# Kernel tuning notes

Hardware: AMD Instinct MI355X
Metric: run time of the kernel (lower is better)

The kernel has to match this reference:

```python
import jax, jax.numpy as jnp
import numpy as np

B, A, G = 16, 32, 512      # batch, atoms, g_feat_in
S, M = 1024, 8             # subset samples, peaks per subset
E, OH = 5, 20              # element types, thermometer size per element
FE = E * OH                # formula encoding = 100
D = 512                    # internal_d
NBINS = 512                # spect bins
EPS = 1e-4


def _ln(x, g, b):
    m = x.mean(-1, keepdims=True)
    v = jnp.mean((x - m) ** 2, -1, keepdims=True)
    return (x - m) * jax.lax.rsqrt(v + 1e-5) * g + b


def setup_inputs() -> dict:
    key = jax.random.key(0)
    ks = jax.random.split(key, 16)
    vert_feat_in = jax.random.normal(ks[0], (B, A, G), jnp.float32)
    vert_mask_in = jnp.ones((B, A), jnp.float32)
    elem = jax.random.randint(ks[1], (B, A), 0, E)
    vert_element_oh = jax.nn.one_hot(elem, E, dtype=jnp.float32)
    atom_subsets = jax.random.randint(ks[2], (B, S, A), 0, 2).astype(jnp.int32)
    atom_subsets_peaks_mass_idx = jax.random.randint(ks[3], (B, S, M), 0, NBINS).astype(jnp.int32)
    atom_subsets_peaks_intensity = jax.random.uniform(ks[4], (B, S, M), jnp.float32)

    def lin(k, o, i):
        s = 1.0 / np.sqrt(i)
        return jax.random.uniform(k, (o, i), jnp.float32, -s, s)

    return dict(
        vert_feat_in=vert_feat_in, vert_mask_in=vert_mask_in,
        vert_element_oh=vert_element_oh, atom_subsets=atom_subsets,
        atom_subsets_peaks_mass_idx=atom_subsets_peaks_mass_idx,
        atom_subsets_peaks_intensity=atom_subsets_peaks_intensity,
        ln_sub_g=jnp.ones((G,)), ln_sub_b=jnp.zeros((G,)),
        W_ih=lin(ks[5], 3 * G, FE), W_hh=lin(ks[6], 3 * G, G),
        b_ih=jnp.zeros((3 * G,)), b_hh=jnp.zeros((3 * G,)),
        ln_post_g=jnp.ones((G,)), ln_post_b=jnp.zeros((G,)),
        W1=lin(ks[7], D, G), b1=jnp.zeros((D,)),
        W2a=lin(ks[8], D, D), b2a=jnp.zeros((D,)),
        W2b=lin(ks[9], D, D), b2b=jnp.zeros((D,)),
        ln_pre_g=jnp.ones((D,)), ln_pre_b=jnp.zeros((D,)),
        W_s=lin(ks[10], 1, D), b_s=jnp.zeros((1,)),
    )


def reference(vert_feat_in, vert_mask_in, vert_element_oh, atom_subsets,
              atom_subsets_peaks_mass_idx, atom_subsets_peaks_intensity,
              ln_sub_g, ln_sub_b, W_ih, W_hh, b_ih, b_hh,
              ln_post_g, ln_post_b, W1, b1, W2a, b2a, W2b, b2b,
              ln_pre_g, ln_pre_b, W_s, b_s):
    subs_f = atom_subsets.astype(jnp.float32)
    masked_vert = vert_feat_in * vert_mask_in[:, :, None]          # B,A,G
    subs_masked = subs_f * vert_mask_in[:, None, :]                 # B,S,A
    # subset-weighted pooling of vertex features
    swv_sum = jnp.einsum('baf,bsa->bsf', masked_vert, subs_masked)  # B,S,G
    subset_size = subs_masked.sum(-1) + EPS                         # B,S
    swv_mean = swv_sum / subset_size[..., None]
    h = _ln(swv_mean, ln_sub_g, ln_sub_b)                           # B,S,G
    # formula counts -> thermometer (accumulating) one-hot; .byte() cast kills grads
    counts = jax.lax.stop_gradient(
        jnp.einsum('bae,bsa->bse', vert_element_oh, subs_f))        # B,S,E
    therm = (jnp.arange(OH, dtype=jnp.float32)[None, None, None, :] < counts[..., None])
    formulae = therm.astype(jnp.float32).reshape(counts.shape[0], counts.shape[1], FE)
    # GRUCell: input=formula encoding, hidden=subset_normed
    gi = jnp.einsum('bsf,gf->bsg', formulae, W_ih) + b_ih           # B,S,3G
    gh = jnp.einsum('bsh,gh->bsg', h, W_hh) + b_hh
    gi_r, gi_z, gi_n = jnp.split(gi, 3, axis=-1)
    gh_r, gh_z, gh_n = jnp.split(gh, 3, axis=-1)
    r = jax.nn.sigmoid(gi_r + gh_r)
    z = jax.nn.sigmoid(gi_z + gh_z)
    n = jnp.tanh(gi_n + r * gh_n)
    combined = (1.0 - z) * n + z * h                                # B,S,G
    x = _ln(combined, ln_post_g, ln_post_b)
    x = jax.nn.relu(jnp.einsum('bsg,dg->bsd', x, W1) + b1)
    x = jax.nn.relu(jnp.einsum('bsd,ed->bse', x, W2a) + b2a)
    x = jax.nn.relu(jnp.einsum('bsd,ed->bse', x, W2b) + b2b)
    x = _ln(x, ln_pre_g, ln_pre_b)
    scores = (jnp.einsum('bsd,od->bso', x, W_s) + b_s)[..., 0]      # B,S
    probs = jax.nn.softmax(scores, axis=-1)                         # B,S
    # sparse mass-matrix multiply: scatter subset probs into spectrum bins
    weighted = atom_subsets_peaks_intensity * probs[:, :, None]     # B,S,M
    bidx = jnp.arange(probs.shape[0])[:, None, None]
    spect_out = jnp.zeros((probs.shape[0], NBINS), probs.dtype)
    spect_out = spect_out.at[bidx, atom_subsets_peaks_mass_idx].add(weighted)
    return spect_out, probs
```

## Files before the change

kernel.cpp:

```cpp
#include <hip/hip_runtime.h>

#define NB 16
#define NA 32
#define NG 512
#define NS 1024
#define NM 8
#define NE 5
#define NOH 20
#define NFE 100
#define ND 512
#define NBINS 512
#define NTOK (NB * NS)

typedef unsigned short ushort_t;
typedef __attribute__((ext_vector_type(8))) short bf16x8;
typedef __attribute__((ext_vector_type(4))) float f32x4;

__device__ __forceinline__ ushort_t f2bf(float x) {
  union { float f; unsigned u; } v; v.f = x;
  unsigned r = v.u + 0x7FFF + ((v.u >> 16) & 1);
  return (ushort_t)(r >> 16);
}
__device__ __forceinline__ float bf2f(ushort_t b) {
  union { unsigned u; float f; } v; v.u = ((unsigned)b) << 16;
  return v.f;
}

__device__ __forceinline__ void gload_lds16(const void* g, void* l) {
  __builtin_amdgcn_global_load_lds(
      (const __attribute__((address_space(1))) void*)g,
      (__attribute__((address_space(3))) void*)l, 16, 0, 0);
}

__device__ __forceinline__ float wsum64(float v) {
#pragma unroll
  for (int off = 32; off > 0; off >>= 1) v += __shfl_xor(v, off);
  return v;
}

__device__ __forceinline__ float fsig(float x) {
  return __builtin_amdgcn_rcpf(1.f + __expf(-x));
}
__device__ __forceinline__ float ftanh(float x) {
  float t = fminf(fmaxf(x, -15.f), 15.f);
  return 1.f - 2.f * __builtin_amdgcn_rcpf(__expf(2.f * t) + 1.f);
}

__global__ __launch_bounds__(256) void setup_kernel(
    const float* __restrict__ vert, const float* __restrict__ mask,
    const float* __restrict__ eloh, const int* __restrict__ subs,
    const float* __restrict__ Wih, const float* __restrict__ Whh,
    const float* __restrict__ W1, const float* __restrict__ W2a,
    const float* __restrict__ W2b,
    float* __restrict__ tcd, float* __restrict__ PS,
    ushort_t* __restrict__ o_hh, ushort_t* __restrict__ o1,
    ushort_t* __restrict__ o2a, ushort_t* __restrict__ o2b,
    ushort_t* __restrict__ VmT, ushort_t* __restrict__ S_bf) {
  int i = blockIdx.x * 256 + threadIdx.x;
  if (i < NTOK) {
    int b = i >> 10;
    const int* srow = subs + (size_t)i * NA;
    float cnt[NE] = {0.f, 0.f, 0.f, 0.f, 0.f};
    float z = 0.f;
    for (int a = 0; a < NA; a++) {
      float sb = (float)srow[a];
      z += sb * mask[b * NA + a];
      const float* eo = eloh + (size_t)(b * NA + a) * NE;
#pragma unroll
      for (int e = 0; e < NE; e++) cnt[e] += eo[e] * sb;
    }
    float* o = tcd + (size_t)i * 8;
#pragma unroll
    for (int e = 0; e < NE; e++) o[e] = cnt[e];
    o[5] = 1.0f / (z + 1e-4f);
    return;
  }
  i -= NTOK;
  if (i < NE * 1536) {
    int e = i / 1536, g = i % 1536;
    float s = 0.f;
    float* base = PS + ((size_t)e * 21) * 1536 + g;
    base[0] = 0.f;
    for (int c = 1; c <= NOH; c++) {
      s += Wih[(size_t)g * NFE + e * NOH + (c - 1)];
      base[(size_t)c * 1536] = s;
    }
    return;
  }
  i -= NE * 1536;
  if (i < 1536 * NG) { o_hh[i] = f2bf(Whh[i]); return; }
  i -= 1536 * NG;
  if (i < ND * NG) { o1[i] = f2bf(W1[i]); return; }
  i -= ND * NG;
  if (i < ND * ND) { o2a[i] = f2bf(W2a[i]); return; }
  i -= ND * ND;
  if (i < ND * ND) { o2b[i] = f2bf(W2b[i]); return; }
  i -= ND * ND;
  const int nV = NB * NG * NA;
  if (i < nV) {
    int b = i / (NG * NA); int rem = i % (NG * NA);
    int f = rem >> 5, a = rem & 31;
    float mk = mask[b * NA + a];
    VmT[i] = f2bf(vert[(size_t)b * NA * NG + a * NG + f] * mk * mk);
    return;
  }
  i -= nV;
  if (i < NTOK * NA) S_bf[i] = f2bf((float)subs[i]);
}

__global__ __launch_bounds__(256) void pool_gemm(
    const ushort_t* __restrict__ S_bf, const ushort_t* __restrict__ VmT,
    const float* __restrict__ tcd, float* __restrict__ SWV, int tok0) {
  __shared__ ushort_t As[128 * 32];
  __shared__ ushort_t Bs[128 * 32];
  const int t = threadIdx.x;
  const int w = t >> 6, lane = t & 63;
  const int wr = w >> 1, wc = w & 1;
  const int bm = blockIdx.x * 128;
  const int bn = blockIdx.y * 128;
  const int b = (tok0 + bm) >> 10;
  const int srow = lane >> 2;
  const int scol = (((lane & 3) ^ ((lane >> 3) & 3)) * 8);
  const ushort_t* Bbase = VmT + (size_t)b * NG * NA;
  gload_lds16(S_bf + (size_t)(tok0 + bm + w * 16 + srow) * 32 + scol, &As[w * 512]);
  gload_lds16(S_bf + (size_t)(tok0 + bm + 64 + w * 16 + srow) * 32 + scol, &As[2048 + w * 512]);
  gload_lds16(Bbase + (size_t)(bn + w * 16 + srow) * 32 + scol, &Bs[w * 512]);
  gload_lds16(Bbase + (size_t)(bn + 64 + w * 16 + srow) * 32 + scol, &Bs[2048 + w * 512]);
  __syncthreads();

  const int lr = lane & 15, lq = lane >> 4;
  const int rchunk = (lq ^ ((lr >> 1) & 3)) * 8;
  f32x4 acc[4][4];
#pragma unroll
  for (int m = 0; m < 4; m++)
#pragma unroll
    for (int n = 0; n < 4; n++) acc[m][n] = (f32x4)0.f;
  bf16x8 a[4], bb[4];
#pragma unroll
  for (int m = 0; m < 4; m++)
    a[m] = *(const bf16x8*)&As[(wr * 64 + m * 16 + lr) * 32 + rchunk];
#pragma unroll
  for (int n = 0; n < 4; n++)
    bb[n] = *(const bf16x8*)&Bs[(wc * 64 + n * 16 + lr) * 32 + rchunk];
#pragma unroll
  for (int m = 0; m < 4; m++)
#pragma unroll
    for (int n = 0; n < 4; n++)
      acc[m][n] = __builtin_amdgcn_mfma_f32_16x16x32_bf16(a[m], bb[n], acc[m][n], 0, 0, 0);

#pragma unroll
  for (int n = 0; n < 4; n++) {
    const int col = bn + wc * 64 + n * 16 + lr;
#pragma unroll
    for (int m = 0; m < 4; m++) {
      f32x4 v = acc[m][n];
#pragma unroll
      for (int r = 0; r < 4; r++) {
        int row = bm + wr * 64 + m * 16 + lq * 4 + r;
        float inv = tcd[(size_t)(tok0 + row) * 8 + 5];
        SWV[(size_t)row * NG + col] = v[r] * inv;
      }
    }
  }
}

__global__ __launch_bounds__(256) void finish_kernel(
    const float* __restrict__ SWV, const float* __restrict__ lng,
    const float* __restrict__ lnb, ushort_t* __restrict__ Hb) {
  const int t = threadIdx.x;
  const int lane = t & 63, wv = t >> 6;
  const int ltok = blockIdx.x * 4 + wv;
  const int f = lane * 8;
  const float* row = SWV + (size_t)ltok * NG + f;
  float4 v0 = *(const float4*)row;
  float4 v1 = *(const float4*)(row + 4);
  float x[8] = {v0.x, v0.y, v0.z, v0.w, v1.x, v1.y, v1.z, v1.w};
  float ps = 0.f;
#pragma unroll
  for (int j = 0; j < 8; j++) ps += x[j];
  float mean = wsum64(ps) * (1.0f / NG);
  float pq = 0.f;
#pragma unroll
  for (int j = 0; j < 8; j++) { float d = x[j] - mean; pq += d * d; }
  float rstd = rsqrtf(wsum64(pq) * (1.0f / NG) + 1e-5f);
  float4 g0 = *(const float4*)&lng[f], g1 = *(const float4*)&lng[f + 4];
  float4 b0 = *(const float4*)&lnb[f], b1 = *(const float4*)&lnb[f + 4];
  float gg[8] = {g0.x, g0.y, g0.z, g0.w, g1.x, g1.y, g1.z, g1.w};
  float bbv[8] = {b0.x, b0.y, b0.z, b0.w, b1.x, b1.y, b1.z, b1.w};
  bf16x8 ho;
#pragma unroll
  for (int j = 0; j < 8; j++) ho[j] = (short)f2bf((x[j] - mean) * rstd * gg[j] + bbv[j]);
  *(bf16x8*)&Hb[(size_t)ltok * NG + f] = ho;
}

__global__ __launch_bounds__(256) void gemm_bf16(
    const ushort_t* __restrict__ A, const ushort_t* __restrict__ W,
    const float* __restrict__ bias, ushort_t* __restrict__ C,
    int K, int Dout, int mode) {
  __shared__ ushort_t As[2][4096];
  __shared__ ushort_t Bs[2][4096];
  const int t = threadIdx.x;
  const int w = t >> 6;
  const int lane = t & 63;
  const int wr = w >> 1, wc = w & 1;
  const int bm = blockIdx.x * 128, bn = blockIdx.y * 128;

  const int srow = lane >> 2;
  const int scol = (((lane & 3) ^ ((lane >> 3) & 3)) * 8);
  const ushort_t* Ag0 = A + (size_t)(bm + w * 16 + srow) * K + scol;
  const ushort_t* Ag1 = A + (size_t)(bm + 64 + w * 16 + srow) * K + scol;
  const ushort_t* Wg0 = W + (size_t)(bn + w * 16 + srow) * K + scol;
  const ushort_t* Wg1 = W + (size_t)(bn + 64 + w * 16 + srow) * K + scol;
  const int l0 = w * 512;
  const int l1 = 2048 + w * 512;

  const int lr = lane & 15;
  const int lq = lane >> 4;
  const int rchunk = (lq ^ ((lr >> 1) & 3)) * 8;

  f32x4 acc[4][4];
#pragma unroll
  for (int m = 0; m < 4; m++)
#pragma unroll
    for (int n = 0; n < 4; n++) acc[m][n] = (f32x4)0.f;

  gload_lds16(Ag0, &As[0][l0]);
  gload_lds16(Ag1, &As[0][l1]);
  gload_lds16(Wg0, &Bs[0][l0]);
  gload_lds16(Wg1, &Bs[0][l1]);
  __syncthreads();

  const int nk = K >> 5;
  int cur = 0;
  for (int kt = 0; kt < nk; kt++) {
    if (kt + 1 < nk) {
      const int k1 = (kt + 1) << 5;
      gload_lds16(Ag0 + k1, &As[cur ^ 1][l0]);
      gload_lds16(Ag1 + k1, &As[cur ^ 1][l1]);
      gload_lds16(Wg0 + k1, &Bs[cur ^ 1][l0]);
      gload_lds16(Wg1 + k1, &Bs[cur ^ 1][l1]);
    }
    bf16x8 a[4], b[4];
#pragma unroll
    for (int m = 0; m < 4; m++)
      a[m] = *(const bf16x8*)&As[cur][(wr * 64 + m * 16 + lr) * 32 + rchunk];
#pragma unroll
    for (int n = 0; n < 4; n++)
      b[n] = *(const bf16x8*)&Bs[cur][(wc * 64 + n * 16 + lr) * 32 + rchunk];
#pragma unroll
    for (int m = 0; m < 4; m++)
#pragma unroll
      for (int n = 0; n < 4; n++)
        acc[m][n] = __builtin_amdgcn_mfma_f32_16x16x32_bf16(a[m], b[n], acc[m][n], 0, 0, 0);
    __syncthreads();
    cur ^= 1;
  }

  ushort_t* sc = (w < 2) ? &As[w][0] : &Bs[w - 2][0];
#pragma unroll
  for (int n = 0; n < 4; n++) {
    const float bv = bias[bn + wc * 64 + n * 16 + lr];
#pragma unroll
    for (int m = 0; m < 4; m++) {
      f32x4 v = acc[m][n];
#pragma unroll
      for (int r = 0; r < 4; r++) {
        const int row = m * 16 + lq * 4 + r;
        float u = v[r] + bv;
        if (mode == 1) u = fmaxf(u, 0.f);
        sc[row * 64 + ((n * 16 + lr) ^ ((row & 7) << 3))] = f2bf(u);
      }
    }
  }
  __builtin_amdgcn_s_waitcnt(0);
#pragma unroll
  for (int p = 0; p < 8; p++) {
    const int row = p * 8 + (lane >> 3);
    bf16x8 pk = *(const bf16x8*)&sc[row * 64 + (((lane & 7) * 8) ^ ((row & 7) << 3))];
    *(bf16x8*)&C[(size_t)(bm + wr * 64 + row) * Dout + bn + wc * 64 + (lane & 7) * 8] = pk;
  }
}

__global__ __launch_bounds__(256) void gate_ln_kernel(
    const ushort_t* __restrict__ Gh, const ushort_t* __restrict__ Hb,
    const float* __restrict__ tcd, const float* __restrict__ PS,
    const float* __restrict__ b_ih, const float* __restrict__ lng,
    const float* __restrict__ lnb, ushort_t* __restrict__ X0) {
  const int t = threadIdx.x;
  const int lane = t & 63, wv = t >> 6;
  const int ltok = blockIdx.x * 4 + wv;
  const int f = lane * 8;
  int c[NE];
#pragma unroll
  for (int e = 0; e < NE; e++) {
    int ci = (int)tcd[(size_t)ltok * 8 + e];
    c[e] = ci > NOH ? NOH : ci;
  }
  float4 r0 = *(const float4*)&b_ih[f],          r1 = *(const float4*)&b_ih[f + 4];
  float4 z0 = *(const float4*)&b_ih[NG + f],     z1 = *(const float4*)&b_ih[NG + f + 4];
  float4 n0 = *(const float4*)&b_ih[2 * NG + f], n1 = *(const float4*)&b_ih[2 * NG + f + 4];
#pragma unroll
  for (int e = 0; e < NE; e++) {
    const float* pe = PS + ((size_t)(e * 21 + c[e])) * 1536;
    r0 += *(const float4*)&pe[f];          r1 += *(const float4*)&pe[f + 4];
    z0 += *(const float4*)&pe[NG + f];     z1 += *(const float4*)&pe[NG + f + 4];
    n0 += *(const float4*)&pe[2 * NG + f]; n1 += *(const float4*)&pe[2 * NG + f + 4];
  }
  float gir[8] = {r0.x, r0.y, r0.z, r0.w, r1.x, r1.y, r1.z, r1.w};
  float giz[8] = {z0.x, z0.y, z0.z, z0.w, z1.x, z1.y, z1.z, z1.w};
  float gin[8] = {n0.x, n0.y, n0.z, n0.w, n1.x, n1.y, n1.z, n1.w};

  const ushort_t* gh = Gh + (size_t)ltok * 1536;
  bf16x8 vr = *(const bf16x8*)&gh[f];
  bf16x8 vz = *(const bf16x8*)&gh[NG + f];
  bf16x8 vn = *(const bf16x8*)&gh[2 * NG + f];
  bf16x8 vh = *(const bf16x8*)&Hb[(size_t)ltok * NG + f];
  float cv[8];
  float ps = 0.f;
#pragma unroll
  for (int j = 0; j < 8; j++) {
    float rg = fsig(gir[j] + bf2f((ushort_t)vr[j]));
    float zg = fsig(giz[j] + bf2f((ushort_t)vz[j]));
    float ng = ftanh(gin[j] + rg * bf2f((ushort_t)vn[j]));
    cv[j] = (1.f - zg) * ng + zg * bf2f((ushort_t)vh[j]);
    ps += cv[j];
  }
  float mean = wsum64(ps) * (1.0f / NG);
  float pq = 0.f;
#pragma unroll
  for (int j = 0; j < 8; j++) { float d = cv[j] - mean; pq += d * d; }
  float rstd = rsqrtf(wsum64(pq) * (1.0f / NG) + 1e-5f);
  float4 g0 = *(const float4*)&lng[f], g1 = *(const float4*)&lng[f + 4];
  float4 b0 = *(const float4*)&lnb[f], b1 = *(const float4*)&lnb[f + 4];
  float gg[8] = {g0.x, g0.y, g0.z, g0.w, g1.x, g1.y, g1.z, g1.w};
  float bbv[8] = {b0.x, b0.y, b0.z, b0.w, b1.x, b1.y, b1.z, b1.w};
  bf16x8 xo;
#pragma unroll
  for (int j = 0; j < 8; j++) xo[j] = (short)f2bf((cv[j] - mean) * rstd * gg[j] + bbv[j]);
  *(bf16x8*)&X0[(size_t)ltok * NG + f] = xo;
}

__global__ __launch_bounds__(256) void ln_score_kernel(
    const ushort_t* __restrict__ X, const float* __restrict__ lng,
    const float* __restrict__ lnb, const float* __restrict__ Wsc,
    const float* __restrict__ bsc, float* __restrict__ scores) {
  const int t = threadIdx.x;
  const int lane = t & 63, wv = t >> 6;
  const int ltok = blockIdx.x * 4 + wv;
  const int f = lane * 8;
  bf16x8 xx = *(const bf16x8*)&X[(size_t)ltok * ND + f];
  float x[8];
  float ps = 0.f;
#pragma unroll
  for (int j = 0; j < 8; j++) { x[j] = bf2f((ushort_t)xx[j]); ps += x[j]; }
  float mean = wsum64(ps) * (1.0f / ND);
  float pq = 0.f;
#pragma unroll
  for (int j = 0; j < 8; j++) { float d = x[j] - mean; pq += d * d; }
  float rstd = rsqrtf(wsum64(pq) * (1.0f / ND) + 1e-5f);
  float4 g0 = *(const float4*)&lng[f], g1 = *(const float4*)&lng[f + 4];
  float4 b0 = *(const float4*)&lnb[f], b1 = *(const float4*)&lnb[f + 4];
  float4 w0 = *(const float4*)&Wsc[f], w1 = *(const float4*)&Wsc[f + 4];
  float gg[8] = {g0.x, g0.y, g0.z, g0.w, g1.x, g1.y, g1.z, g1.w};
  float bbv[8] = {b0.x, b0.y, b0.z, b0.w, b1.x, b1.y, b1.z, b1.w};
  float ww[8] = {w0.x, w0.y, w0.z, w0.w, w1.x, w1.y, w1.z, w1.w};
  float d = 0.f;
#pragma unroll
  for (int j = 0; j < 8; j++) d += ((x[j] - mean) * rstd * gg[j] + bbv[j]) * ww[j];
  float dot = wsum64(d);
  if (lane == 0) scores[ltok] = dot + bsc[0];
}

__global__ __launch_bounds__(256) void softmax_scatter_kernel(
    const float* __restrict__ scores, const int* __restrict__ pidx,
    const float* __restrict__ pint, float* __restrict__ spect,
    float* __restrict__ probs) {
  const int b = blockIdx.x;
  const int t = threadIdx.x;
  __shared__ float s_red[4];
  __shared__ float s_spec[NBINS];
  const float* sc = scores + (size_t)b * NS;
  float v[4];
  float mx = -1e30f;
#pragma unroll
  for (int i = 0; i < 4; i++) { v[i] = sc[t + i * 256]; mx = fmaxf(mx, v[i]); }
#pragma unroll
  for (int off = 32; off > 0; off >>= 1) mx = fmaxf(mx, __shfl_down(mx, off));
  if ((t & 63) == 0) s_red[t >> 6] = mx;
  __syncthreads();
  mx = fmaxf(fmaxf(s_red[0], s_red[1]), fmaxf(s_red[2], s_red[3]));
  float e[4], sum = 0.f;
#pragma unroll
  for (int i = 0; i < 4; i++) { e[i] = expf(v[i] - mx); sum += e[i]; }
#pragma unroll
  for (int off = 32; off > 0; off >>= 1) sum += __shfl_down(sum, off);
  __syncthreads();
  if ((t & 63) == 0) s_red[t >> 6] = sum;
  __syncthreads();
  sum = s_red[0] + s_red[1] + s_red[2] + s_red[3];
  float inv = 1.f / sum;
  s_spec[t] = 0.f; s_spec[t + 256] = 0.f;
  float p[4];
#pragma unroll
  for (int i = 0; i < 4; i++) {
    p[i] = e[i] * inv;
    probs[(size_t)b * NS + t + i * 256] = p[i];
  }
  __syncthreads();
#pragma unroll
  for (int i = 0; i < 4; i++) {
    const int s = t + i * 256;
    const int* idx = pidx + ((size_t)b * NS + s) * NM;
    const float* wt = pint + ((size_t)b * NS + s) * NM;
#pragma unroll
    for (int m = 0; m < NM; m++)
      atomicAdd(&s_spec[idx[m]], wt[m] * p[i]);
  }
  __syncthreads();
  spect[(size_t)b * NBINS + t] = s_spec[t];
  spect[(size_t)b * NBINS + t + 256] = s_spec[t + 256];
}

extern "C" void kernel_launch(void* const* d_in, const int* in_sizes, int n_in,
                              void* d_out, int out_size, void* d_ws, size_t ws_size,
                              hipStream_t stream) {
  const float* vert = (const float*)d_in[0];
  const float* mask = (const float*)d_in[1];
  const float* eloh = (const float*)d_in[2];
  const int* subs = (const int*)d_in[3];
  const int* pidx = (const int*)d_in[4];
  const float* pint = (const float*)d_in[5];
  const float* ln_sub_g = (const float*)d_in[6];
  const float* ln_sub_b = (const float*)d_in[7];
  const float* W_ih = (const float*)d_in[8];
  const float* W_hh = (const float*)d_in[9];
  const float* b_ih = (const float*)d_in[10];
  const float* b_hh = (const float*)d_in[11];
  const float* ln_post_g = (const float*)d_in[12];
  const float* ln_post_b = (const float*)d_in[13];
  const float* W1 = (const float*)d_in[14];
  const float* b1 = (const float*)d_in[15];
  const float* W2a = (const float*)d_in[16];
  const float* b2a = (const float*)d_in[17];
  const float* W2b = (const float*)d_in[18];
  const float* b2b = (const float*)d_in[19];
  const float* ln_pre_g = (const float*)d_in[20];
  const float* ln_pre_b = (const float*)d_in[21];
  const float* W_s = (const float*)d_in[22];
  const float* b_s = (const float*)d_in[23];

  float* out = (float*)d_out;
  float* probs = out + NB * NBINS;

  char* ws = (char*)d_ws;
  float* scores = (float*)ws;
  ushort_t* Whh_bf = (ushort_t*)(ws + 65536);
  ushort_t* W1_bf  = (ushort_t*)(ws + 1638400);
  ushort_t* W2a_bf = (ushort_t*)(ws + 2162688);
  ushort_t* W2b_bf = (ushort_t*)(ws + 2686976);
  ushort_t* VmT    = (ushort_t*)(ws + 3211264);
  ushort_t* S_bf   = (ushort_t*)(ws + 3735552);
  float*    tcd    = (float*)(ws + 4784128);
  float*    PS     = (float*)(ws + 5308416);
  const size_t fixed = 5953536;

  const size_t per_tok = 7168;
  int T = NTOK;
  while (T > 1024 && fixed + (size_t)T * per_tok > ws_size) T >>= 1;
  const int nchunks = NTOK / T;

  char* cb = ws + fixed;
  float*    SWV = (float*)cb;                             cb += (size_t)T * 2048;
  ushort_t* Hb  = (ushort_t*)cb;                          cb += (size_t)T * 1024;
  ushort_t* Gh  = (ushort_t*)cb;                          cb += (size_t)T * 3072;
  ushort_t* X0  = (ushort_t*)cb;
  ushort_t* X1  = Gh;
  ushort_t* X2  = Gh + (size_t)T * 512;
  ushort_t* X3  = X0;

  const int setup_items = NTOK + NE * 1536 + 1536 * NG + ND * NG + 2 * ND * ND
                        + NB * NG * NA + NTOK * NA;
  setup_kernel<<<(setup_items + 255) / 256, 256, 0, stream>>>(
      vert, mask, eloh, subs, W_ih, W_hh, W1, W2a, W2b,
      tcd, PS, Whh_bf, W1_bf, W2a_bf, W2b_bf, VmT, S_bf);

  for (int c = 0; c < nchunks; c++) {
    const int tok0 = c * T;

    dim3 gp(T / 128, NG / 128);
    pool_gemm<<<gp, 256, 0, stream>>>(S_bf, VmT, tcd, SWV, tok0);
    finish_kernel<<<T / 4, 256, 0, stream>>>(SWV, ln_sub_g, ln_sub_b, Hb);

    dim3 g1(T / 128, 1536 / 128);
    gemm_bf16<<<g1, 256, 0, stream>>>(Hb, Whh_bf, b_hh, Gh, NG, 1536, 3);

    gate_ln_kernel<<<T / 4, 256, 0, stream>>>(Gh, Hb, tcd + (size_t)tok0 * 8, PS,
                                              b_ih, ln_post_g, ln_post_b, X0);

    dim3 g2(T / 128, ND / 128);
    gemm_bf16<<<g2, 256, 0, stream>>>(X0, W1_bf, b1, X1, NG, ND, 1);
    gemm_bf16<<<g2, 256, 0, stream>>>(X1, W2a_bf, b2a, X2, ND, ND, 1);
    gemm_bf16<<<g2, 256, 0, stream>>>(X2, W2b_bf, b2b, X3, ND, ND, 1);

    ln_score_kernel<<<T / 4, 256, 0, stream>>>(X3, ln_pre_g, ln_pre_b, W_s, b_s,
                                               scores + tok0);
  }

  softmax_scatter_kernel<<<NB, 256, 0, stream>>>(scores, pidx, pint, out, probs);
}
```

Measured before the change: 263.4 us.

## Fuse three FFN GEMMs and final LayerNorm-score into one LDS-resident kernel

Replaces the three separate bf16 GEMM launches and the ln_score kernel with a single kernel. Each 512-thread block keeps a 64-token activation tile in two swizzled LDS buffers and runs all three 512x512 layers back to back, with MFMA operands read from LDS and weights streamed from global memory. The final LayerNorm and score dot product are computed from LDS. This removes the global round trips of the intermediate activations and three launches. The cost is 128KB of LDS per block, so only one block fits per CU, and T/64 blocks may give low occupancy with weights reloaded by every block.

Measured after the change: 264.5 us. No clear change (+0.4%).

```diff
diff --git a/kernel.cpp b/kernel.cpp
--- a/kernel.cpp
+++ b/kernel.cpp
@@ -340,35 +340,106 @@
   *(bf16x8*)&X0[(size_t)ltok * NG + f] = xo;
 }
 
-__global__ __launch_bounds__(256) void ln_score_kernel(
-    const ushort_t* __restrict__ X, const float* __restrict__ lng,
+__device__ __forceinline__ void ffn_layer(
+    const ushort_t* src, ushort_t* dst, const ushort_t* __restrict__ Wl,
+    const float* __restrict__ bl, const int w, const int lane) {
+  const int lr = lane & 15, lq = lane >> 4;
+  const int cw = w * 64;
+  const int sw = lr & 7;
+  f32x4 acc[4][4];
+#pragma unroll
+  for (int m = 0; m < 4; m++)
+#pragma unroll
+    for (int n = 0; n < 4; n++) acc[m][n] = (f32x4)0.f;
+  const ushort_t* wp0 = Wl + (size_t)(cw + 0 + lr) * 512 + lq * 8;
+  const ushort_t* wp1 = Wl + (size_t)(cw + 16 + lr) * 512 + lq * 8;
+  const ushort_t* wp2 = Wl + (size_t)(cw + 32 + lr) * 512 + lq * 8;
+  const ushort_t* wp3 = Wl + (size_t)(cw + 48 + lr) * 512 + lq * 8;
+#pragma unroll
+  for (int kt = 0; kt < 16; kt++) {
+    bf16x8 a[4], b[4];
+    const int ch = (kt * 4 + lq) ^ sw;
+#pragma unroll
+    for (int m = 0; m < 4; m++)
+      a[m] = *(const bf16x8*)&src[(m * 16 + lr) * 512 + ch * 8];
+    b[0] = *(const bf16x8*)(wp0 + kt * 32);
+    b[1] = *(const bf16x8*)(wp1 + kt * 32);
+    b[2] = *(const bf16x8*)(wp2 + kt * 32);
+    b[3] = *(const bf16x8*)(wp3 + kt * 32);
+#pragma unroll
+    for (int m = 0; m < 4; m++)
+#pragma unroll
+      for (int n = 0; n < 4; n++)
+        acc[m][n] = __builtin_amdgcn_mfma_f32_16x16x32_bf16(a[m], b[n], acc[m][n], 0, 0, 0);
+  }
+#pragma unroll
+  for (int n = 0; n < 4; n++) {
+    const int c = cw + n * 16 + lr;
+    const float bv = bl[c];
+#pragma unroll
+    for (int m = 0; m < 4; m++) {
+      f32x4 v = acc[m][n];
+#pragma unroll
+      for (int r = 0; r < 4; r++) {
+        const int row = m * 16 + lq * 4 + r;
+        float u = fmaxf(v[r] + bv, 0.f);
+        dst[row * 512 + (((c >> 3) ^ (row & 7)) << 3) + (c & 7)] = f2bf(u);
+      }
+    }
+  }
+}
+
+__global__ __launch_bounds__(512) void ffn_kernel(
+    const ushort_t* __restrict__ X0g, const ushort_t* __restrict__ W1l,
+    const float* __restrict__ b1l, const ushort_t* __restrict__ W2al,
+    const float* __restrict__ b2al, const ushort_t* __restrict__ W2bl,
+    const float* __restrict__ b2bl, const float* __restrict__ lng,
     const float* __restrict__ lnb, const float* __restrict__ Wsc,
-    const float* __restrict__ bsc, float* __restrict__ scores) {
+    const float* __restrict__ bsc, float* __restrict__ scores, int tok0) {
+  __shared__ ushort_t Xa[64 * 512];
+  __shared__ ushort_t Xb[64 * 512];
   const int t = threadIdx.x;
-  const int lane = t & 63, wv = t >> 6;
-  const int ltok = blockIdx.x * 4 + wv;
-  const int f = lane * 8;
-  bf16x8 xx = *(const bf16x8*)&X[(size_t)ltok * ND + f];
-  float x[8];
-  float ps = 0.f;
-#pragma unroll
-  for (int j = 0; j < 8; j++) { x[j] = bf2f((ushort_t)xx[j]); ps += x[j]; }
-  float mean = wsum64(ps) * (1.0f / ND);
-  float pq = 0.f;
-#pragma unroll
-  for (int j = 0; j < 8; j++) { float d = x[j] - mean; pq += d * d; }
-  float rstd = rsqrtf(wsum64(pq) * (1.0f / ND) + 1e-5f);
-  float4 g0 = *(const float4*)&lng[f], g1 = *(const float4*)&lng[f + 4];
-  float4 b0 = *(const float4*)&lnb[f], b1 = *(const float4*)&lnb[f + 4];
-  float4 w0 = *(const float4*)&Wsc[f], w1 = *(const float4*)&Wsc[f + 4];
-  float gg[8] = {g0.x, g0.y, g0.z, g0.w, g1.x, g1.y, g1.z, g1.w};
-  float bbv[8] = {b0.x, b0.y, b0.z, b0.w, b1.x, b1.y, b1.z, b1.w};
-  float ww[8] = {w0.x, w0.y, w0.z, w0.w, w1.x, w1.y, w1.z, w1.w};
-  float d = 0.f;
-#pragma unroll
-  for (int j = 0; j < 8; j++) d += ((x[j] - mean) * rstd * gg[j] + bbv[j]) * ww[j];
-  float dot = wsum64(d);
-  if (lane == 0) scores[ltok] = dot + bsc[0];
+  const int w = t >> 6, lane = t & 63;
+  const int tb = blockIdx.x * 64;
+#pragma unroll
+  for (int i = 0; i < 8; i++) {
+    const int row = i * 8 + w;
+    gload_lds16(X0g + (size_t)(tok0 + tb + row) * 512 + ((lane ^ w) << 3),
+                &Xa[i * 4096 + w * 512]);
+  }
+  __syncthreads();
+  ffn_layer(Xa, Xb, W1l, b1l, w, lane);
+  __syncthreads();
+  ffn_layer(Xb, Xa, W2al, b2al, w, lane);
+  __syncthreads();
+  ffn_layer(Xa, Xb, W2bl, b2bl, w, lane);
+  __syncthreads();
+#pragma unroll
+  for (int j = 0; j < 8; j++) {
+    const int row = w * 8 + j;
+    bf16x8 xx = *(const bf16x8*)&Xb[row * 512 + ((lane ^ (row & 7)) << 3)];
+    float x[8];
+    float ps = 0.f;
+#pragma unroll
+    for (int q = 0; q < 8; q++) { x[q] = bf2f((ushort_t)xx[q]); ps += x[q]; }
+    float mean = wsum64(ps) * (1.0f / ND);
+    float pq = 0.f;
+#pragma unroll
+    for (int q = 0; q < 8; q++) { float d = x[q] - mean; pq += d * d; }
+    float rstd = rsqrtf(wsum64(pq) * (1.0f / ND) + 1e-5f);
+    const int f = lane * 8;
+    float4 g0 = *(const float4*)&lng[f], g1 = *(const float4*)&lng[f + 4];
+    float4 e0 = *(const float4*)&lnb[f], e1 = *(const float4*)&lnb[f + 4];
+    float4 s0 = *(const float4*)&Wsc[f], s1 = *(const float4*)&Wsc[f + 4];
+    float gg[8] = {g0.x, g0.y, g0.z, g0.w, g1.x, g1.y, g1.z, g1.w};
+    float bv[8] = {e0.x, e0.y, e0.z, e0.w, e1.x, e1.y, e1.z, e1.w};
+    float ww[8] = {s0.x, s0.y, s0.z, s0.w, s1.x, s1.y, s1.z, s1.w};
+    float d = 0.f;
+#pragma unroll
+    for (int q = 0; q < 8; q++) d += ((x[q] - mean) * rstd * gg[q] + bv[q]) * ww[q];
+    float dot = wsum64(d);
+    if (lane == 0) scores[tok0 + tb + row] = dot + bsc[0];
+  }
 }
 
 __global__ __launch_bounds__(256) void softmax_scatter_kernel(
@@ -474,9 +545,6 @@
   ushort_t* Hb  = (ushort_t*)cb;                          cb += (size_t)T * 1024;
   ushort_t* Gh  = (ushort_t*)cb;                          cb += (size_t)T * 3072;
   ushort_t* X0  = (ushort_t*)cb;
-  ushort_t* X1  = Gh;
-  ushort_t* X2  = Gh + (size_t)T * 512;
-  ushort_t* X3  = X0;
 
   const int setup_items = NTOK + NE * 1536 + 1536 * NG + ND * NG + 2 * ND * ND
                         + NB * NG * NA + NTOK * NA;
@@ -497,13 +565,8 @@
     gate_ln_kernel<<<T / 4, 256, 0, stream>>>(Gh, Hb, tcd + (size_t)tok0 * 8, PS,
                                               b_ih, ln_post_g, ln_post_b, X0);
 
-    dim3 g2(T / 128, ND / 128);
-    gemm_bf16<<<g2, 256, 0, stream>>>(X0, W1_bf, b1, X1, NG, ND, 1);
-    gemm_bf16<<<g2, 256, 0, stream>>>(X1, W2a_bf, b2a, X2, ND, ND, 1);
-    gemm_bf16<<<g2, 256, 0, stream>>>(X2, W2b_bf, b2b, X3, ND, ND, 1);
-
-    ln_score_kernel<<<T / 4, 256, 0, stream>>>(X3, ln_pre_g, ln_pre_b, W_s, b_s,
-                                               scores + tok0);
+    ffn_kernel<<<T / 64, 512, 0, stream>>>(X0, W1_bf, b1, W2a_bf, b2a, W2b_bf, b2b,
+                                           ln_pre_g, ln_pre_b, W_s, b_s, scores, tok0);
   }
 
   softmax_scatter_kernel<<<NB, 256, 0, stream>>>(scores, pidx, pint, out, probs);
```
